# Performance work log

Hardware: AMD Instinct MI355X
Metric: run time of the kernel (lower is better)

Reference implementation:

```python
import jax, jax.numpy as jnp
import numpy as np

K = 1254  # top-k patches kept by the gate


def setup_inputs() -> dict:
    key = jax.random.key(0)
    k1, k2 = jax.random.split(key)
    x = jax.random.normal(k1, (16, 224, 224, 64), dtype=jnp.float32)
    gating_kernel = jax.random.normal(k2, (2, 2, 64, 1), dtype=jnp.float32) * 0.05
    return {"x": x, "gating_kernel": gating_kernel}


def reference(x, gating_kernel):
    # x: [B, H, W, C] (NHWC), gating_kernel: [kh, kw, C, 1]
    B, H, W, C = x.shape
    kh, kw = gating_kernel.shape[0], gating_kernel.shape[1]
    # 1-channel gating conv, stride == kernel size, 'valid' padding -> [B, Ho, Wo]
    g = jax.lax.conv_general_dilated(
        x, gating_kernel,
        window_strides=(kh, kw), padding='VALID',
        dimension_numbers=('NHWC', 'HWIO', 'NHWC'))[..., 0]
    Ho, Wo = g.shape[1], g.shape[2]
    n = Ho * Wo
    flat = g.reshape(B, n)
    # top-k patch scores per image; activation is linear (None) in this config
    values, indices = jax.lax.top_k(flat, K)
    # scatter-sum values back to a dense [B, n] gate (top_k indices are distinct,
    # so add == unsorted_segment_sum exactly)
    batch_idx = jnp.arange(B)[:, None]  # [B, 1]
    gate = jnp.zeros((B, n), dtype=x.dtype).at[batch_idx, indices].add(values)
    gate = gate.reshape(B, Ho, Wo)
    # broadcast each patch score over its kh x kw spatial block and all C channels
    gate_full = jnp.broadcast_to(
        gate[:, :, None, :, None], (B, Ho, kh, Wo, kw)).reshape(B, H, W)
    return x * gate_full[..., None]
```

## Files before the change

kernel.cpp:

```cpp
#include <hip/hip_runtime.h>
#include <hip/hip_bf16.h>
#include <stdint.h>

#define BATCH   16
#define HDIM    224
#define WDIM    224
#define CDIM    64
#define HO      112
#define WO      112
#define NPATCH  (HO * WO)
#define KSEL    1254
#define ROWF    (WDIM * CDIM)
#define PERTHR  49
#define ROWF4   (WDIM * 16)
#define BLKROW  14

typedef float f32x4 __attribute__((ext_vector_type(4)));

__global__ __launch_bounds__(256) void conv_gate_kernel(
    const float* __restrict__ x, const float* __restrict__ wk,
    float* __restrict__ g) {
  const int tid = threadIdx.x;
  const int lane = tid & 31;
  const int p = blockIdx.x * 8 + (tid >> 5);

  const int b   = p / NPATCH;
  const int rem = p - b * NPATCH;
  const int ho  = rem / WO;
  const int wo  = rem - ho * WO;

  const float4 w0 = *reinterpret_cast<const float4*>(wk + lane * 4);
  const float4 w1 = *reinterpret_cast<const float4*>(wk + 128 + lane * 4);

  const long row0 = (long)(b * HDIM + 2 * ho) * ROWF + wo * 128 + lane * 4;
  const float4 a0 = *reinterpret_cast<const float4*>(x + row0);
  const float4 a1 = *reinterpret_cast<const float4*>(x + row0 + ROWF);

  float partial = a0.x * w0.x + a0.y * w0.y + a0.z * w0.z + a0.w * w0.w
                + a1.x * w1.x + a1.y * w1.y + a1.z * w1.z + a1.w * w1.w;

  #pragma unroll
  for (int off = 16; off > 0; off >>= 1)
    partial += __shfl_down(partial, off, 32);

  if (lane == 0) g[p] = partial;
}

__global__ __launch_bounds__(256) void select_kernel(
    const float* __restrict__ g, float* __restrict__ gate) {
  __shared__ int cnt[2][4];
  __shared__ int eq_list[256];
  __shared__ int eq_count;

  const int b = blockIdx.x;
  const int tid = threadIdx.x;
  const float* __restrict__ gb  = g    + b * NPATCH;
  float* __restrict__       gtb = gate + b * NPATCH;

  uint32_t key[PERTHR];
  #pragma unroll
  for (int j = 0; j < PERTHR; ++j) {
    uint32_t u = __float_as_uint(gb[tid + j * 256]);
    key[j] = (u & 0x80000000u) ? ~u : (u | 0x80000000u);
  }
  if (tid == 0) eq_count = 0;

  int par = 0;
  auto block_count = [&](int c) -> int {
    #pragma unroll
    for (int off = 32; off > 0; off >>= 1) c += __shfl_down(c, off, 64);
    if ((tid & 63) == 0) cnt[par][tid >> 6] = c;
    __syncthreads();
    const int tot = cnt[par][0] + cnt[par][1] + cnt[par][2] + cnt[par][3];
    par ^= 1;
    return tot;
  };

  uint32_t T = 0;
  for (int bit = 31; bit >= 0; --bit) {
    const uint32_t cand = T | (1u << bit);
    int c = 0;
    #pragma unroll
    for (int j = 0; j < PERTHR; ++j) c += (key[j] >= cand) ? 1 : 0;
    if (block_count(c) >= KSEL) T = cand;
  }

  int cg = 0;
  #pragma unroll
  for (int j = 0; j < PERTHR; ++j) cg += (key[j] > T) ? 1 : 0;
  const int krem = KSEL - block_count(cg);

  #pragma unroll
  for (int j = 0; j < PERTHR; ++j) {
    const int i = tid + j * 256;
    const uint32_t k = key[j];
    float v = 0.0f;
    if (k > T) {
      uint32_t u = (k & 0x80000000u) ? (k & 0x7FFFFFFFu) : ~k;
      v = __uint_as_float(u);
    }
    gtb[i] = v;
    if (k == T) {
      int pos = atomicAdd(&eq_count, 1);
      if (pos < 256) eq_list[pos] = i;
    }
  }
  __syncthreads();

  if (tid == 0) {
    const int ec = eq_count;
    const float tval =
        __uint_as_float((T & 0x80000000u) ? (T & 0x7FFFFFFFu) : ~T);
    if (ec <= 256) {
      for (int i = 0; i < ec; ++i) {
        int mn = i;
        for (int j = i + 1; j < ec; ++j)
          if (eq_list[j] < eq_list[mn]) mn = j;
        int t = eq_list[mn]; eq_list[mn] = eq_list[i]; eq_list[i] = t;
      }
      for (int i = 0; i < ec && i < krem; ++i)
        gtb[eq_list[i]] = tval;
    } else {
      int kept = 0;
      for (int i = 0; i < NPATCH && kept < krem; ++i) {
        uint32_t u = __float_as_uint(gb[i]);
        uint32_t k = (u & 0x80000000u) ? ~u : (u | 0x80000000u);
        if (k == T) { gtb[i] = tval; ++kept; }
      }
    }
  }
}

__global__ __launch_bounds__(256) void apply_gate_kernel(
    const float* __restrict__ x, const float* __restrict__ gate,
    float* __restrict__ out) {
  const int bi = blockIdx.x;
  const int rowblk = bi % BLKROW;
  const int rowid  = bi / BLKROW;
  const int h = rowid % HDIM;
  const int b = rowid / HDIM;

  const int v4row = rowblk * 256 + threadIdx.x;
  const int w = v4row >> 4;
  const int gidx = b * NPATCH + (h >> 1) * WO + (w >> 1);

  const float gv = gate[gidx];
  const size_t v4 = (size_t)rowid * ROWF4 + v4row;

  f32x4 o = {0.0f, 0.0f, 0.0f, 0.0f};
  if (gv != 0.0f) {
    const f32x4 a = *reinterpret_cast<const f32x4*>(x + v4 * 4);
    o = a * gv;
  }
  __builtin_nontemporal_store(o, reinterpret_cast<f32x4*>(out + v4 * 4));
}

extern "C" void kernel_launch(void* const* d_in, const int* in_sizes, int n_in,
                              void* d_out, int out_size, void* d_ws, size_t ws_size,
                              hipStream_t stream) {
  const float* x  = (const float*)d_in[0];
  const float* wk = (const float*)d_in[1];
  float* out = (float*)d_out;

  float* g    = (float*)d_ws;
  float* gate = g + BATCH * NPATCH;

  conv_gate_kernel<<<(BATCH * NPATCH) / 8, 256, 0, stream>>>(x, wk, g);
  select_kernel<<<BATCH, 256, 0, stream>>>(g, gate);
  apply_gate_kernel<<<BATCH * HDIM * BLKROW, 256, 0, stream>>>(x, gate, out);
}
```

Measured before the change: 354.6 us.

## Compact selected patches into a list and zero output concurrently with selection

The selection kernel now emits a compact list of (patch index, value) pairs using wave ballots instead of a dense gate array. Extra blocks in the same launch write zeros over the whole output while the 16 selection blocks run. A new apply kernel then processes only the selected patches, one wave per patch, reading x and writing scaled output. This removes the dense gate lookup pass and overlaps the zero-fill with the serial top-k, at the cost of scattered small accesses and an ordering dependence between the zero writes and the later patch writes.

```diff
diff --git a/kernel.cpp b/kernel.cpp
--- a/kernel.cpp
+++ b/kernel.cpp
@@ -1,5 +1,4 @@
 #include <hip/hip_runtime.h>
-#include <hip/hip_bf16.h>
 #include <stdint.h>
 
 #define BATCH   16
@@ -13,7 +12,10 @@
 #define ROWF    (WDIM * CDIM)
 #define PERTHR  49
 #define ROWF4   (WDIM * 16)
-#define BLKROW  14
+#define OUTV4   (BATCH * HDIM * ROWF4)
+#define ZBLK    3136
+#define ZPT     16
+#define NSELTOT (BATCH * KSEL)
 
 typedef float f32x4 __attribute__((ext_vector_type(4)));
 
@@ -46,16 +48,30 @@
   if (lane == 0) g[p] = partial;
 }
 
-__global__ __launch_bounds__(256) void select_kernel(
-    const float* __restrict__ g, float* __restrict__ gate) {
+__global__ __launch_bounds__(256) void select_zero_kernel(
+    const float* __restrict__ g, uint2* __restrict__ list,
+    float* __restrict__ out) {
+  const int tid = threadIdx.x;
+
+  if (blockIdx.x >= 16) {
+    const int base = (blockIdx.x - 16) * 256 + tid;
+    const f32x4 z = {0.0f, 0.0f, 0.0f, 0.0f};
+    f32x4* o = reinterpret_cast<f32x4*>(out);
+    #pragma unroll
+    for (int k = 0; k < ZPT; ++k)
+      __builtin_nontemporal_store(z, o + base + (size_t)k * (ZBLK * 256));
+    return;
+  }
+
   __shared__ int cnt[2][4];
   __shared__ int eq_list[256];
   __shared__ int eq_count;
+  __shared__ int nsel;
 
   const int b = blockIdx.x;
-  const int tid = threadIdx.x;
-  const float* __restrict__ gb  = g    + b * NPATCH;
-  float* __restrict__       gtb = gate + b * NPATCH;
+  const int lane = tid & 63;
+  const float* __restrict__ gb = g + b * NPATCH;
+  uint2* __restrict__ lb = list + b * KSEL;
 
   uint32_t key[PERTHR];
   #pragma unroll
@@ -63,7 +79,7 @@
     uint32_t u = __float_as_uint(gb[tid + j * 256]);
     key[j] = (u & 0x80000000u) ? ~u : (u | 0x80000000u);
   }
-  if (tid == 0) eq_count = 0;
+  if (tid == 0) { eq_count = 0; nsel = 0; }
 
   int par = 0;
   auto block_count = [&](int c) -> int {
@@ -94,12 +110,16 @@
   for (int j = 0; j < PERTHR; ++j) {
     const int i = tid + j * 256;
     const uint32_t k = key[j];
-    float v = 0.0f;
-    if (k > T) {
-      uint32_t u = (k & 0x80000000u) ? (k & 0x7FFFFFFFu) : ~k;
-      v = __uint_as_float(u);
+    const bool sel = (k > T);
+    const unsigned long long m = __ballot(sel);
+    int base;
+    if (lane == 0) base = atomicAdd(&nsel, __popcll(m));
+    base = __shfl(base, 0, 64);
+    if (sel) {
+      const int pos = base + __popcll(m & ((1ull << lane) - 1ull));
+      const uint32_t u = (k & 0x80000000u) ? (k & 0x7FFFFFFFu) : ~k;
+      lb[pos] = make_uint2((uint32_t)i, u);
     }
-    gtb[i] = v;
     if (k == T) {
       int pos = atomicAdd(&eq_count, 1);
       if (pos < 256) eq_list[pos] = i;
@@ -109,8 +129,8 @@
 
   if (tid == 0) {
     const int ec = eq_count;
-    const float tval =
-        __uint_as_float((T & 0x80000000u) ? (T & 0x7FFFFFFFu) : ~T);
+    const int base2 = KSEL - krem;
+    const uint32_t tbits = (T & 0x80000000u) ? (T & 0x7FFFFFFFu) : ~T;
     if (ec <= 256) {
       for (int i = 0; i < ec; ++i) {
         int mn = i;
@@ -119,39 +139,37 @@
         int t = eq_list[mn]; eq_list[mn] = eq_list[i]; eq_list[i] = t;
       }
       for (int i = 0; i < ec && i < krem; ++i)
-        gtb[eq_list[i]] = tval;
+        lb[base2 + i] = make_uint2((uint32_t)eq_list[i], tbits);
     } else {
       int kept = 0;
       for (int i = 0; i < NPATCH && kept < krem; ++i) {
         uint32_t u = __float_as_uint(gb[i]);
         uint32_t k = (u & 0x80000000u) ? ~u : (u | 0x80000000u);
-        if (k == T) { gtb[i] = tval; ++kept; }
+        if (k == T) { lb[base2 + kept] = make_uint2((uint32_t)i, tbits); ++kept; }
       }
     }
   }
 }
 
-__global__ __launch_bounds__(256) void apply_gate_kernel(
-    const float* __restrict__ x, const float* __restrict__ gate,
+__global__ __launch_bounds__(256) void apply_list_kernel(
+    const float* __restrict__ x, const uint2* __restrict__ list,
     float* __restrict__ out) {
-  const int bi = blockIdx.x;
-  const int rowblk = bi % BLKROW;
-  const int rowid  = bi / BLKROW;
-  const int h = rowid % HDIM;
-  const int b = rowid / HDIM;
+  const int wid = blockIdx.x * 4 + (threadIdx.x >> 6);
+  const int lane = threadIdx.x & 63;
 
-  const int v4row = rowblk * 256 + threadIdx.x;
-  const int w = v4row >> 4;
-  const int gidx = b * NPATCH + (h >> 1) * WO + (w >> 1);
+  const uint2 ent = list[wid];
+  const int b   = wid / KSEL;
+  const int idx = (int)ent.x;
+  const float val = __uint_as_float(ent.y);
 
-  const float gv = gate[gidx];
-  const size_t v4 = (size_t)rowid * ROWF4 + v4row;
+  const int ho = idx / WO;
+  const int wo = idx - ho * WO;
+  const size_t base_v4 = (size_t)(b * HDIM + 2 * ho) * ROWF4 + wo * 32;
+  const size_t v4 = base_v4 + (lane < 32 ? (size_t)lane
+                                         : (size_t)(ROWF4 + lane - 32));
 
-  f32x4 o = {0.0f, 0.0f, 0.0f, 0.0f};
-  if (gv != 0.0f) {
-    const f32x4 a = *reinterpret_cast<const f32x4*>(x + v4 * 4);
-    o = a * gv;
-  }
+  const f32x4 a = *reinterpret_cast<const f32x4*>(x + v4 * 4);
+  const f32x4 o = a * val;
   __builtin_nontemporal_store(o, reinterpret_cast<f32x4*>(out + v4 * 4));
 }
 
@@ -163,9 +181,9 @@
   float* out = (float*)d_out;
 
   float* g    = (float*)d_ws;
-  float* gate = g + BATCH * NPATCH;
+  uint2* list = (uint2*)((char*)d_ws + (size_t)BATCH * NPATCH * 4);
 
   conv_gate_kernel<<<(BATCH * NPATCH) / 8, 256, 0, stream>>>(x, wk, g);
-  select_kernel<<<BATCH, 256, 0, stream>>>(g, gate);
-  apply_gate_kernel<<<BATCH * HDIM * BLKROW, 256, 0, stream>>>(x, gate, out);
+  select_zero_kernel<<<16 + ZBLK, 256, 0, stream>>>(g, list, out);
+  apply_list_kernel<<<NSELTOT / 4, 256, 0, stream>>>(x, list, out);
 }
```

New measurement: 343.6 us (median of 2 runs). 1.03x faster.
